# Optimization experiments

Measured on AMD Instinct MI355X. Metric: run time of the kernel, lower is better.

## Reference

```python
import jax, jax.numpy as jnp
import numpy as np

N, C, M = 100000, 1024, 128


def setup_inputs() -> dict:
    key = jax.random.key(0)
    k1, k2, k3, k4, k5, k6, k7 = jax.random.split(key, 7)
    return {
        "class_scores": jax.random.uniform(k1, (N, C), dtype=jnp.float32),
        "xywh": jax.random.normal(k2, (N, 4), dtype=jnp.float32),
        "z": jax.random.uniform(k3, (N,), dtype=jnp.float32),
        "r": jax.random.uniform(k4, (N,), dtype=jnp.float32),
        "nearest_gt_idx": jax.random.randint(k5, (N,), 0, M, dtype=jnp.int32),
        "gt_class_labels": jax.random.randint(k6, (M,), 0, C, dtype=jnp.int32),
        "gt_xywh": jax.random.normal(k7, (M, 4), dtype=jnp.float32),
    }


def reference(class_scores, xywh, z, r, nearest_gt_idx, gt_class_labels, gt_xywh):
    # class_scores are detached in the original tpc/fpc loops
    cs = jax.lax.stop_gradient(class_scores)  # [N, C]
    labels = gt_class_labels[nearest_gt_idx]  # [N] label of nearest GT per detection
    # zero out the nearest-GT class column per row, then row-max + log
    col = jnp.arange(cs.shape[1], dtype=labels.dtype)[None, :]
    masked = jnp.where(col == labels[:, None], jnp.zeros((), cs.dtype), cs)
    log_max = jnp.log(jnp.max(masked, axis=1))  # [N]
    tpc = -jnp.sum(z * log_max)
    fpc = -jnp.sum(r * log_max)
    # shape loss: exp(-sum_i z_i * ||xywh_i - gt_xywh[nearest_i]||^2)
    dist = jnp.sum((xywh - gt_xywh[nearest_gt_idx]) ** 2, axis=1)  # [N]
    tps = jnp.exp(-jnp.sum(z * dist))
    return jnp.reshape(tpc + tps + fpc, (1,))
```

## Files before the change

kernel.cpp:

```cpp
#include <hip/hip_runtime.h>
#include <math.h>

#define NROWS 100000
#define CCOLS 1024
#define GRID  2048
#define BLOCK 256
#define WPB   (BLOCK / 64)

__global__ __launch_bounds__(BLOCK) void bp_main(
    const float* __restrict__ cs,
    const float* __restrict__ xywh,
    const float* __restrict__ z,
    const float* __restrict__ r,
    const int*   __restrict__ nearest,
    const int*   __restrict__ gt_lbl,
    const float* __restrict__ gt_xywh,
    float* __restrict__ partials,
    int n)
{
    const int lane  = threadIdx.x & 63;
    const int wave  = threadIdx.x >> 6;
    const int gwave = blockIdx.x * WPB + wave;
    const int nwav  = gridDim.x * WPB;

    float acc_z = 0.f, acc_r = 0.f, acc_d = 0.f;

    for (int row = gwave; row < n; row += nwav) {
        const int   gi    = nearest[row];
        const int   label = gt_lbl[gi];
        const float4* rowp = (const float4*)(cs + (size_t)row * CCOLS);

        float m = 0.f;
        #pragma unroll
        for (int k = 0; k < 4; ++k) {
            const int    idx   = lane + k * 64;
            const int    cbase = idx * 4;
            const float4 v     = rowp[idx];
            const float a = (cbase + 0 == label) ? 0.f : v.x;
            const float b = (cbase + 1 == label) ? 0.f : v.y;
            const float c = (cbase + 2 == label) ? 0.f : v.z;
            const float d = (cbase + 3 == label) ? 0.f : v.w;
            m = fmaxf(m, fmaxf(fmaxf(a, b), fmaxf(c, d)));
        }
        #pragma unroll
        for (int off = 32; off >= 1; off >>= 1)
            m = fmaxf(m, __shfl_xor(m, off, 64));

        if (lane == 0) {
            const float lm = logf(m);
            const float zi = z[row];
            const float ri = r[row];
            const float4 x = *(const float4*)(xywh    + (size_t)row * 4);
            const float4 g = *(const float4*)(gt_xywh + (size_t)gi  * 4);
            const float dx = x.x - g.x, dy = x.y - g.y,
                        dw = x.z - g.z, dh = x.w - g.w;
            const float dist = dx * dx + dy * dy + dw * dw + dh * dh;
            acc_z += zi * lm;
            acc_r += ri * lm;
            acc_d += zi * dist;
        }
    }

    __shared__ float s[WPB][3];
    if (lane == 0) { s[wave][0] = acc_z; s[wave][1] = acc_r; s[wave][2] = acc_d; }
    __syncthreads();
    if (threadIdx.x == 0) {
        float sz = 0.f, sr = 0.f, sd = 0.f;
        #pragma unroll
        for (int w = 0; w < WPB; ++w) { sz += s[w][0]; sr += s[w][1]; sd += s[w][2]; }
        partials[            blockIdx.x] = sz;
        partials[    GRID +  blockIdx.x] = sr;
        partials[2 * GRID +  blockIdx.x] = sd;
    }
}

__global__ __launch_bounds__(256) void bp_final(
    const float* __restrict__ partials, float* __restrict__ out)
{
    float sz = 0.f, sr = 0.f, sd = 0.f;
    for (int i = threadIdx.x; i < GRID; i += 256) {
        sz += partials[i];
        sr += partials[GRID + i];
        sd += partials[2 * GRID + i];
    }
    #pragma unroll
    for (int off = 32; off >= 1; off >>= 1) {
        sz += __shfl_xor(sz, off, 64);
        sr += __shfl_xor(sr, off, 64);
        sd += __shfl_xor(sd, off, 64);
    }
    __shared__ float sh[4][3];
    const int lane = threadIdx.x & 63;
    const int wave = threadIdx.x >> 6;
    if (lane == 0) { sh[wave][0] = sz; sh[wave][1] = sr; sh[wave][2] = sd; }
    __syncthreads();
    if (threadIdx.x == 0) {
        float tz = 0.f, tr = 0.f, td = 0.f;
        #pragma unroll
        for (int w = 0; w < 4; ++w) { tz += sh[w][0]; tr += sh[w][1]; td += sh[w][2]; }
        out[0] = -tz - tr + expf(-td);
    }
}

extern "C" void kernel_launch(void* const* d_in, const int* in_sizes, int n_in,
                              void* d_out, int out_size, void* d_ws, size_t ws_size,
                              hipStream_t stream) {
    const float* cs      = (const float*)d_in[0];
    const float* xywh    = (const float*)d_in[1];
    const float* z       = (const float*)d_in[2];
    const float* r       = (const float*)d_in[3];
    const int*   nearest = (const int*)  d_in[4];
    const int*   gt_lbl  = (const int*)  d_in[5];
    const float* gt_xywh = (const float*)d_in[6];
    float* out = (float*)d_out;
    float* partials = (float*)d_ws;
    const int n = in_sizes[2];

    bp_main<<<GRID, BLOCK, 0, stream>>>(cs, xywh, z, r, nearest, gt_lbl,
                                        gt_xywh, partials, n);
    bp_final<<<1, 256, 0, stream>>>(partials, out);
}
```

Before: 78.52 us.

## Fuse final reduction via last-block atomic and process two rows per wave

Merges the separate final-reduction kernel into the main kernel using a global atomic counter so the last block sums the partials, which removes one kernel launch. Each wave now handles two rows at a time, so two rows' loads are in flight together, and the log and distance tail is spread across both half-waves. The grid is halved to 1024 blocks. A memset of the counter is added on the stream, which may cost about as much as the launch it replaces.

```diff
diff --git a/kernel.cpp b/kernel.cpp
--- a/kernel.cpp
+++ b/kernel.cpp
@@ -1,13 +1,12 @@
 #include <hip/hip_runtime.h>
 #include <math.h>
 
-#define NROWS 100000
 #define CCOLS 1024
-#define GRID  2048
+#define GRID  1024
 #define BLOCK 256
 #define WPB   (BLOCK / 64)
 
-__global__ __launch_bounds__(BLOCK) void bp_main(
+__global__ __launch_bounds__(BLOCK) void bp_fused(
     const float* __restrict__ cs,
     const float* __restrict__ xywh,
     const float* __restrict__ z,
@@ -15,7 +14,9 @@
     const int*   __restrict__ nearest,
     const int*   __restrict__ gt_lbl,
     const float* __restrict__ gt_xywh,
-    float* __restrict__ partials,
+    float*        __restrict__ partials,
+    unsigned int* __restrict__ counter,
+    float*        __restrict__ out,
     int n)
 {
     const int lane  = threadIdx.x & 63;
@@ -25,43 +26,94 @@
 
     float acc_z = 0.f, acc_r = 0.f, acc_d = 0.f;
 
-    for (int row = gwave; row < n; row += nwav) {
-        const int   gi    = nearest[row];
-        const int   label = gt_lbl[gi];
-        const float4* rowp = (const float4*)(cs + (size_t)row * CCOLS);
+    int row0 = gwave * 2;
+    const int stride = nwav * 2;
 
-        float m = 0.f;
+    for (; row0 + 1 < n; row0 += stride) {
+        const int rowA = row0, rowB = row0 + 1;
+        const int giA = nearest[rowA], giB = nearest[rowB];
+        const int lbA = gt_lbl[giA],   lbB = gt_lbl[giB];
+        const float4* pA = (const float4*)(cs + (size_t)rowA * CCOLS);
+        const float4* pB = (const float4*)(cs + (size_t)rowB * CCOLS);
+
+        float mA = 0.f, mB = 0.f;
         #pragma unroll
         for (int k = 0; k < 4; ++k) {
             const int    idx   = lane + k * 64;
             const int    cbase = idx * 4;
-            const float4 v     = rowp[idx];
-            const float a = (cbase + 0 == label) ? 0.f : v.x;
-            const float b = (cbase + 1 == label) ? 0.f : v.y;
-            const float c = (cbase + 2 == label) ? 0.f : v.z;
-            const float d = (cbase + 3 == label) ? 0.f : v.w;
-            m = fmaxf(m, fmaxf(fmaxf(a, b), fmaxf(c, d)));
+            const float4 vA = pA[idx];
+            const float4 vB = pB[idx];
+            const float a0 = (cbase + 0 == lbA) ? 0.f : vA.x;
+            const float a1 = (cbase + 1 == lbA) ? 0.f : vA.y;
+            const float a2 = (cbase + 2 == lbA) ? 0.f : vA.z;
+            const float a3 = (cbase + 3 == lbA) ? 0.f : vA.w;
+            const float b0 = (cbase + 0 == lbB) ? 0.f : vB.x;
+            const float b1 = (cbase + 1 == lbB) ? 0.f : vB.y;
+            const float b2 = (cbase + 2 == lbB) ? 0.f : vB.z;
+            const float b3 = (cbase + 3 == lbB) ? 0.f : vB.w;
+            mA = fmaxf(mA, fmaxf(fmaxf(a0, a1), fmaxf(a2, a3)));
+            mB = fmaxf(mB, fmaxf(fmaxf(b0, b1), fmaxf(b2, b3)));
         }
         #pragma unroll
-        for (int off = 32; off >= 1; off >>= 1)
-            m = fmaxf(m, __shfl_xor(m, off, 64));
+        for (int off = 32; off >= 1; off >>= 1) {
+            mA = fmaxf(mA, __shfl_xor(mA, off, 64));
+            mB = fmaxf(mB, __shfl_xor(mB, off, 64));
+        }
 
-        if (lane == 0) {
-            const float lm = logf(m);
-            const float zi = z[row];
-            const float ri = r[row];
-            const float4 x = *(const float4*)(xywh    + (size_t)row * 4);
-            const float4 g = *(const float4*)(gt_xywh + (size_t)gi  * 4);
-            const float dx = x.x - g.x, dy = x.y - g.y,
-                        dw = x.z - g.z, dh = x.w - g.w;
-            const float dist = dx * dx + dy * dy + dw * dw + dh * dh;
+        const int   rowsel = (lane & 32) ? rowB : rowA;
+        const int   gisel  = (lane & 32) ? giB  : giA;
+        const float msel   = (lane & 32) ? mB   : mA;
+        const float lm = logf(msel);
+        const float zi = z[rowsel];
+        const float ri = r[rowsel];
+        const float4 x = *(const float4*)(xywh    + (size_t)rowsel * 4);
+        const float4 g = *(const float4*)(gt_xywh + (size_t)gisel  * 4);
+        const float dx = x.x - g.x, dy = x.y - g.y,
+                    dw = x.z - g.z, dh = x.w - g.w;
+        const float dist = dx * dx + dy * dy + dw * dw + dh * dh;
+        if ((lane & 31) == 0) {
             acc_z += zi * lm;
             acc_r += ri * lm;
             acc_d += zi * dist;
         }
     }
 
+    if (row0 < n) {
+        const int gi = nearest[row0];
+        const int lb = gt_lbl[gi];
+        const float4* p = (const float4*)(cs + (size_t)row0 * CCOLS);
+        float m = 0.f;
+        #pragma unroll
+        for (int k = 0; k < 4; ++k) {
+            const int idx = lane + k * 64, cbase = idx * 4;
+            const float4 v = p[idx];
+            const float a = (cbase + 0 == lb) ? 0.f : v.x;
+            const float b = (cbase + 1 == lb) ? 0.f : v.y;
+            const float c = (cbase + 2 == lb) ? 0.f : v.z;
+            const float d = (cbase + 3 == lb) ? 0.f : v.w;
+            m = fmaxf(m, fmaxf(fmaxf(a, b), fmaxf(c, d)));
+        }
+        #pragma unroll
+        for (int off = 32; off >= 1; off >>= 1)
+            m = fmaxf(m, __shfl_xor(m, off, 64));
+        if (lane == 0) {
+            const float lm = logf(m);
+            const float zi = z[row0], ri = r[row0];
+            const float4 x = *(const float4*)(xywh    + (size_t)row0 * 4);
+            const float4 g = *(const float4*)(gt_xywh + (size_t)gi   * 4);
+            const float dx = x.x - g.x, dy = x.y - g.y,
+                        dw = x.z - g.z, dh = x.w - g.w;
+            acc_z += zi * lm; acc_r += ri * lm;
+            acc_d += zi * (dx*dx + dy*dy + dw*dw + dh*dh);
+        }
+    }
+
+    acc_z += __shfl_xor(acc_z, 32, 64);
+    acc_r += __shfl_xor(acc_r, 32, 64);
+    acc_d += __shfl_xor(acc_d, 32, 64);
+
     __shared__ float s[WPB][3];
+    __shared__ bool  s_last;
     if (lane == 0) { s[wave][0] = acc_z; s[wave][1] = acc_r; s[wave][2] = acc_d; }
     __syncthreads();
     if (threadIdx.x == 0) {
@@ -71,34 +123,35 @@
         partials[            blockIdx.x] = sz;
         partials[    GRID +  blockIdx.x] = sr;
         partials[2 * GRID +  blockIdx.x] = sd;
+        __threadfence();
+        const unsigned t = atomicAdd(counter, 1u);
+        s_last = (t == gridDim.x - 1);
     }
-}
+    __syncthreads();
 
-__global__ __launch_bounds__(256) void bp_final(
-    const float* __restrict__ partials, float* __restrict__ out)
-{
-    float sz = 0.f, sr = 0.f, sd = 0.f;
-    for (int i = threadIdx.x; i < GRID; i += 256) {
-        sz += partials[i];
-        sr += partials[GRID + i];
-        sd += partials[2 * GRID + i];
-    }
-    #pragma unroll
-    for (int off = 32; off >= 1; off >>= 1) {
-        sz += __shfl_xor(sz, off, 64);
-        sr += __shfl_xor(sr, off, 64);
-        sd += __shfl_xor(sd, off, 64);
-    }
-    __shared__ float sh[4][3];
-    const int lane = threadIdx.x & 63;
-    const int wave = threadIdx.x >> 6;
-    if (lane == 0) { sh[wave][0] = sz; sh[wave][1] = sr; sh[wave][2] = sd; }
-    __syncthreads();
-    if (threadIdx.x == 0) {
-        float tz = 0.f, tr = 0.f, td = 0.f;
+    if (s_last) {
+        __threadfence();
+        float sz = 0.f, sr = 0.f, sd = 0.f;
+        for (int i = threadIdx.x; i < GRID; i += BLOCK) {
+            sz += partials[i];
+            sr += partials[GRID + i];
+            sd += partials[2 * GRID + i];
+        }
         #pragma unroll
-        for (int w = 0; w < 4; ++w) { tz += sh[w][0]; tr += sh[w][1]; td += sh[w][2]; }
-        out[0] = -tz - tr + expf(-td);
+        for (int off = 32; off >= 1; off >>= 1) {
+            sz += __shfl_xor(sz, off, 64);
+            sr += __shfl_xor(sr, off, 64);
+            sd += __shfl_xor(sd, off, 64);
+        }
+        __shared__ float sh[WPB][3];
+        if (lane == 0) { sh[wave][0] = sz; sh[wave][1] = sr; sh[wave][2] = sd; }
+        __syncthreads();
+        if (threadIdx.x == 0) {
+            float tz = 0.f, tr = 0.f, td = 0.f;
+            #pragma unroll
+            for (int w = 0; w < WPB; ++w) { tz += sh[w][0]; tr += sh[w][1]; td += sh[w][2]; }
+            out[0] = -tz - tr + expf(-td);
+        }
     }
 }
 
@@ -113,10 +166,13 @@
     const int*   gt_lbl  = (const int*)  d_in[5];
     const float* gt_xywh = (const float*)d_in[6];
     float* out = (float*)d_out;
-    float* partials = (float*)d_ws;
+
+    float*        partials = (float*)d_ws;
+    unsigned int* counter  = (unsigned int*)((char*)d_ws + 3 * GRID * sizeof(float));
     const int n = in_sizes[2];
 
-    bp_main<<<GRID, BLOCK, 0, stream>>>(cs, xywh, z, r, nearest, gt_lbl,
-                                        gt_xywh, partials, n);
-    bp_final<<<1, 256, 0, stream>>>(partials, out);
+    hipMemsetAsync((void*)counter, 0, sizeof(unsigned int), stream);
+
+    bp_fused<<<GRID, BLOCK, 0, stream>>>(cs, xywh, z, r, nearest, gt_lbl,
+                                         gt_xywh, partials, counter, out, n);
 }
```

Result: slower. 125.4 us (+59.8%).
